# Kernel optimization log

Measured on AMD Instinct MI355X. Metric: run time of the kernel, lower is better.

The kernel has to match this reference:

```python
import jax, jax.numpy as jnp
import numpy as np

NUM_NEURON = 500_000
NUM_CONN = 8
SIM_TIME = 200
I_MAX = 20.0
FIRE_THRESHOLD = 0.5
# Izhikevich neuron parameters
THRESHOLD = 30.0
A, B, C_RESET, D = 0.02, 0.2, -65.0, 8.0
MEM0, U0 = -70.0, -14.0
DT = 0.5


def setup_inputs() -> dict:
    key = jax.random.key(0)
    k0, k1, k2, k3, k4 = jax.random.split(key, 5)
    inp = jax.random.uniform(k0, (NUM_NEURON,), jnp.float32)
    FR = jax.random.uniform(k1, (NUM_CONN, NUM_NEURON), jnp.float32)
    C = jax.random.uniform(k2, (NUM_NEURON,), jnp.float32)
    W = jax.random.normal(k3, (NUM_CONN, NUM_NEURON), jnp.float32) * 0.5
    Fired = jnp.ones((1,), jnp.float32)
    W_LatInh = jax.random.normal(k4, (NUM_NEURON,), jnp.float32)
    return {"input": inp, "FR": FR, "C": C, "Fired": Fired,
            "W_LatInh": W_LatInh, "W": W}


def _izh_spike_count(I):
    """Run SIM_TIME Izhikevich steps with constant input current I; return spike counts."""
    def step(carry, _):
        mem, u, acc = carry
        mem = mem + DT * (0.04 * mem * mem + 5.0 * mem + 140.0 - u + I)
        u = u + DT * A * (B * mem - u)
        spike = (mem >= THRESHOLD).astype(I.dtype)
        mem = spike * C_RESET + (1.0 - spike) * mem
        u = u + spike * D
        return (mem, u, acc + spike), None
    mem0 = jnp.full_like(I, MEM0)
    u0 = jnp.full_like(I, U0)
    acc0 = jnp.zeros_like(I)
    (_, _, acc), _ = jax.lax.scan(step, (mem0, u0, acc0), None, length=SIM_TIME)
    return acc


def reference(input, FR, C, Fired, W_LatInh, W):
    # weighted firing-rate sum over all input connections: [K,N] -> [N]
    FR_W = jnp.einsum('kn,kn->n', FR, W)
    sf = jnp.maximum(jnp.tanh(FR_W), 0.0)
    input_n = jnp.maximum(-C * (input - sf) + input, 0.0)
    input_r = jnp.round(input_n * I_MAX)
    spike_count = _izh_spike_count(input_r)
    FR_n = spike_count / SIM_TIME
    # binarize to detect fired neurons
    S = jnp.where(input_n >= FIRE_THRESHOLD, 1.0, 0.0)
    fired_any = (jnp.sum(S) > 0.0).astype(input.dtype)
    Fired_new = Fired + fired_any
    W_cand = jnp.tanh(W_LatInh - 2.0 * jnp.arccos(S) * jnp.exp(Fired_new) - 1.0) + 1.0
    W_LatInh_new = jnp.where(fired_any > 0.0, W_cand, W_LatInh)
    return FR_n, input_n, Fired_new, W_LatInh_new
```

## Files before the change

kernel.cpp:

```cpp
#include <hip/hip_runtime.h>


namespace {

constexpr int N    = 500000;
constexpr int NT4  = N / 4;
constexpr int BLK  = 256;
constexpr int NBLK = (NT4 + BLK - 1) / BLK;

__device__ __forceinline__ float xla_tanh(float x) {
  float xc = fminf(fmaxf(x, -9.0f), 9.0f);
  float x2 = __fmul_rn(xc, xc);
  float p = -2.76076847742355e-16f;
  p = __fadd_rn(__fmul_rn(p, x2), 2.00018790482477e-13f);
  p = __fadd_rn(__fmul_rn(p, x2), -8.60467152213735e-11f);
  p = __fadd_rn(__fmul_rn(p, x2), 5.12229709037114e-08f);
  p = __fadd_rn(__fmul_rn(p, x2), 1.48572235717979e-05f);
  p = __fadd_rn(__fmul_rn(p, x2), 6.37261928875436e-04f);
  p = __fadd_rn(__fmul_rn(p, x2), 4.89352455891786e-03f);
  p = __fmul_rn(xc, p);
  float q = 1.19825839466702e-06f;
  q = __fadd_rn(__fmul_rn(q, x2), 1.18534705686654e-04f);
  q = __fadd_rn(__fmul_rn(q, x2), 2.26843463243900e-03f);
  q = __fadd_rn(__fmul_rn(q, x2), 4.89352518554385e-03f);
  float r = p / q;
  return (fabsf(x) < 0.0004f) ? x : r;
}

__global__ void __launch_bounds__(BLK) kA(const float* __restrict__ inp,
                                          const float* __restrict__ FR,
                                          const float* __restrict__ C,
                                          const float* __restrict__ W,
                                          float* __restrict__ out,
                                          unsigned int* __restrict__ flag) {
  __shared__ float lut[24];
  const int tid = threadIdx.x;
  const int gid = blockIdx.x * BLK + tid;
  const bool active = gid < NT4;
  const int src = active ? gid : 0;

  float4 in4 = reinterpret_cast<const float4*>(inp)[src];
  float4 c4  = reinterpret_cast<const float4*>(C)[src];
  float fa[8][4], wa[8][4];
#pragma unroll
  for (int k = 0; k < 8; ++k) {
    float4 fv = reinterpret_cast<const float4*>(FR + (size_t)k * N)[src];
    float4 wv = reinterpret_cast<const float4*>(W + (size_t)k * N)[src];
    fa[k][0] = fv.x; fa[k][1] = fv.y; fa[k][2] = fv.z; fa[k][3] = fv.w;
    wa[k][0] = wv.x; wa[k][1] = wv.y; wa[k][2] = wv.z; wa[k][3] = wv.w;
  }

  if (tid < 21) {
    const float I = (float)tid;
    float mem = -70.0f, u = -14.0f, acc = 0.0f;
#pragma unroll 10
    for (int t = 0; t < 200; ++t) {
      float dm = (0.04f * mem) * mem + 5.0f * mem;
      dm = dm + 140.0f;
      dm = dm - u;
      dm = dm + I;
      mem = mem + 0.5f * dm;
      u = u + 0.01f * (0.2f * mem - u);
      const bool sp = mem >= 30.0f;
      acc += sp ? 1.0f : 0.0f;
      mem = sp ? -65.0f : mem;
      u = sp ? u + 8.0f : u;
    }
    lut[tid] = acc / 200.0f;
  }
  __syncthreads();

  if (!active) return;

  float frw[4];
#pragma unroll
  for (int j = 0; j < 4; ++j) {
    float s = __fmul_rn(fa[0][j], wa[0][j]);
#pragma unroll
    for (int k = 1; k < 8; ++k)
      s = __fadd_rn(s, __fmul_rn(fa[k][j], wa[k][j]));
    frw[j] = s;
  }

  const float iv[4] = {in4.x, in4.y, in4.z, in4.w};
  const float cv[4] = {c4.x, c4.y, c4.z, c4.w};
  float fr_n[4], in_n[4];
  bool s_any = false;
#pragma unroll
  for (int j = 0; j < 4; ++j) {
    float sf = fmaxf(xla_tanh(frw[j]), 0.0f);
    float d  = __fsub_rn(iv[j], sf);
    float v  = __fadd_rn(__fmul_rn(-cv[j], d), iv[j]);
    float n  = fmaxf(v, 0.0f);
    in_n[j] = n;
    int ir = (int)rintf(__fmul_rn(n, 20.0f));
    ir = ir < 0 ? 0 : (ir > 20 ? 20 : ir);
    fr_n[j] = lut[ir];
    s_any |= (n >= 0.5f);
  }

  float4 o0 = {fr_n[0], fr_n[1], fr_n[2], fr_n[3]};
  float4 o1 = {in_n[0], in_n[1], in_n[2], in_n[3]};
  reinterpret_cast<float4*>(out)[gid] = o0;
  reinterpret_cast<float4*>(out + N)[gid] = o1;

  unsigned long long b = __ballot(s_any);
  if (b != 0ULL && (int)(tid & 63) == (__ffsll((unsigned long long)b) - 1))
    *flag = 1u;
}

__global__ void __launch_bounds__(BLK) kB(const float* __restrict__ WLi,
                                          const float* __restrict__ Fired,
                                          const unsigned int* __restrict__ flag,
                                          float* __restrict__ out) {
  const int gid = blockIdx.x * BLK + threadIdx.x;
  const float fired_any = (*flag != 0u) ? 1.0f : 0.0f;
  const float fired_new = __fadd_rn(Fired[0], fired_any);
  if (gid == 0) out[2 * N] = fired_new;
  if (gid >= NT4) return;

  float4 wl4 = reinterpret_cast<const float4*>(WLi)[gid];
  float4 in4 = reinterpret_cast<const float4*>(out + N)[gid];
  const float wv[4] = {wl4.x, wl4.y, wl4.z, wl4.w};
  const float nv[4] = {in4.x, in4.y, in4.z, in4.w};
  float res[4];

  if (fired_any > 0.0f) {
    const float e = expf(fired_new);
#pragma unroll
    for (int j = 0; j < 4; ++j) {
      float two_acos = (nv[j] >= 0.5f) ? 0.0f : 3.14159274101257324f;
      float t = __fmul_rn(two_acos, e);
      float x = __fsub_rn(wv[j], t);
      x = __fsub_rn(x, 1.0f);
      res[j] = __fadd_rn(xla_tanh(x), 1.0f);
    }
  } else {
#pragma unroll
    for (int j = 0; j < 4; ++j) res[j] = wv[j];
  }

  float* dst = out + 2 * N + 1 + (size_t)gid * 4;
  dst[0] = res[0]; dst[1] = res[1]; dst[2] = res[2]; dst[3] = res[3];
}

}

extern "C" void kernel_launch(void* const* d_in, const int* in_sizes, int n_in,
                              void* d_out, int out_size, void* d_ws, size_t ws_size,
                              hipStream_t stream) {
  const float* inp   = (const float*)d_in[0];
  const float* FR    = (const float*)d_in[1];
  const float* C     = (const float*)d_in[2];
  const float* Fired = (const float*)d_in[3];
  const float* WLi   = (const float*)d_in[4];
  const float* W     = (const float*)d_in[5];
  float* out = (float*)d_out;
  unsigned int* flag = (unsigned int*)d_ws;

  hipMemsetAsync(flag, 0, sizeof(unsigned int), stream);
  kA<<<NBLK, BLK, 0, stream>>>(inp, FR, C, W, out, flag);
  kB<<<NBLK, BLK, 0, stream>>>(WLi, Fired, flag, out);
}
```

Baseline: 99.65 us.

## Fuse both kernels into one cooperative kernel with a grid-wide sync

Merges the main compute kernel and the lateral-inhibition update kernel into a single cooperative launch. Each block writes its own fired flag, then after a grid sync every block ORs all the flags. This removes the memset, the second launch, and the reload of input_n and W_LatInh from global memory, since the values stay in registers across the sync. In exchange it depends on all 489 blocks being co-resident, adds the cost of a grid barrier, and keeps more registers live across that barrier.

```diff
diff --git a/kernel.cpp b/kernel.cpp
--- a/kernel.cpp
+++ b/kernel.cpp
@@ -1,5 +1,8 @@
 #include <hip/hip_runtime.h>
+#include <hip/hip_cooperative_groups.h>
 
+
+namespace cg = cooperative_groups;
 
 namespace {
 
@@ -27,20 +30,27 @@
   return (fabsf(x) < 0.0004f) ? x : r;
 }
 
-__global__ void __launch_bounds__(BLK) kA(const float* __restrict__ inp,
-                                          const float* __restrict__ FR,
-                                          const float* __restrict__ C,
-                                          const float* __restrict__ W,
-                                          float* __restrict__ out,
-                                          unsigned int* __restrict__ flag) {
+__global__ void __launch_bounds__(BLK) kFused(const float* __restrict__ inp,
+                                              const float* __restrict__ FR,
+                                              const float* __restrict__ C,
+                                              const float* __restrict__ W,
+                                              const float* __restrict__ WLi,
+                                              const float* __restrict__ Fired,
+                                              float* __restrict__ out,
+                                              unsigned int* __restrict__ flags) {
   __shared__ float lut[24];
+  __shared__ unsigned int s_or;
   const int tid = threadIdx.x;
-  const int gid = blockIdx.x * BLK + tid;
+  const int bid = blockIdx.x;
+  const int gid = bid * BLK + tid;
   const bool active = gid < NT4;
   const int src = active ? gid : 0;
 
+  if (tid == 0) s_or = 0u;
+
   float4 in4 = reinterpret_cast<const float4*>(inp)[src];
   float4 c4  = reinterpret_cast<const float4*>(C)[src];
+  float4 wl4 = reinterpret_cast<const float4*>(WLi)[src];
   float fa[8][4], wa[8][4];
 #pragma unroll
   for (int k = 0; k < 8; ++k) {
@@ -70,78 +80,77 @@
   }
   __syncthreads();
 
-  if (!active) return;
-
-  float frw[4];
+  float in_n[4];
+  bool s_any = false;
+  if (active) {
+    float frw[4];
 #pragma unroll
-  for (int j = 0; j < 4; ++j) {
-    float s = __fmul_rn(fa[0][j], wa[0][j]);
+    for (int j = 0; j < 4; ++j) {
+      float s = __fmul_rn(fa[0][j], wa[0][j]);
 #pragma unroll
-    for (int k = 1; k < 8; ++k)
-      s = __fadd_rn(s, __fmul_rn(fa[k][j], wa[k][j]));
-    frw[j] = s;
+      for (int k = 1; k < 8; ++k)
+        s = __fadd_rn(s, __fmul_rn(fa[k][j], wa[k][j]));
+      frw[j] = s;
+    }
+    const float iv[4] = {in4.x, in4.y, in4.z, in4.w};
+    const float cv[4] = {c4.x, c4.y, c4.z, c4.w};
+    float fr_n[4];
+#pragma unroll
+    for (int j = 0; j < 4; ++j) {
+      float sf = fmaxf(xla_tanh(frw[j]), 0.0f);
+      float d  = __fsub_rn(iv[j], sf);
+      float v  = __fadd_rn(__fmul_rn(-cv[j], d), iv[j]);
+      float n  = fmaxf(v, 0.0f);
+      in_n[j] = n;
+      int ir = (int)rintf(__fmul_rn(n, 20.0f));
+      ir = ir < 0 ? 0 : (ir > 20 ? 20 : ir);
+      fr_n[j] = lut[ir];
+      s_any |= (n >= 0.5f);
+    }
+    float4 o0 = {fr_n[0], fr_n[1], fr_n[2], fr_n[3]};
+    float4 o1 = {in_n[0], in_n[1], in_n[2], in_n[3]};
+    reinterpret_cast<float4*>(out)[gid] = o0;
+    reinterpret_cast<float4*>(out + N)[gid] = o1;
   }
 
-  const float iv[4] = {in4.x, in4.y, in4.z, in4.w};
-  const float cv[4] = {c4.x, c4.y, c4.z, c4.w};
-  float fr_n[4], in_n[4];
-  bool s_any = false;
-#pragma unroll
-  for (int j = 0; j < 4; ++j) {
-    float sf = fmaxf(xla_tanh(frw[j]), 0.0f);
-    float d  = __fsub_rn(iv[j], sf);
-    float v  = __fadd_rn(__fmul_rn(-cv[j], d), iv[j]);
-    float n  = fmaxf(v, 0.0f);
-    in_n[j] = n;
-    int ir = (int)rintf(__fmul_rn(n, 20.0f));
-    ir = ir < 0 ? 0 : (ir > 20 ? 20 : ir);
-    fr_n[j] = lut[ir];
-    s_any |= (n >= 0.5f);
-  }
+  unsigned long long b = __ballot(s_any);
+  if ((tid & 63) == 0 && b != 0ULL) s_or = 1u;
+  __syncthreads();
+  if (tid == 0) flags[bid] = s_or;
 
-  float4 o0 = {fr_n[0], fr_n[1], fr_n[2], fr_n[3]};
-  float4 o1 = {in_n[0], in_n[1], in_n[2], in_n[3]};
-  reinterpret_cast<float4*>(out)[gid] = o0;
-  reinterpret_cast<float4*>(out + N)[gid] = o1;
+  cg::this_grid().sync();
 
-  unsigned long long b = __ballot(s_any);
-  if (b != 0ULL && (int)(tid & 63) == (__ffsll((unsigned long long)b) - 1))
-    *flag = 1u;
-}
+  unsigned int v = 0;
+  for (int i = tid; i < NBLK; i += BLK) v |= flags[i];
+  if (tid == 0) s_or = 0u;
+  __syncthreads();
+  if (v != 0u) s_or = 1u;
+  __syncthreads();
 
-__global__ void __launch_bounds__(BLK) kB(const float* __restrict__ WLi,
-                                          const float* __restrict__ Fired,
-                                          const unsigned int* __restrict__ flag,
-                                          float* __restrict__ out) {
-  const int gid = blockIdx.x * BLK + threadIdx.x;
-  const float fired_any = (*flag != 0u) ? 1.0f : 0.0f;
+  const float fired_any = s_or ? 1.0f : 0.0f;
   const float fired_new = __fadd_rn(Fired[0], fired_any);
   if (gid == 0) out[2 * N] = fired_new;
-  if (gid >= NT4) return;
 
-  float4 wl4 = reinterpret_cast<const float4*>(WLi)[gid];
-  float4 in4 = reinterpret_cast<const float4*>(out + N)[gid];
-  const float wv[4] = {wl4.x, wl4.y, wl4.z, wl4.w};
-  const float nv[4] = {in4.x, in4.y, in4.z, in4.w};
-  float res[4];
-
-  if (fired_any > 0.0f) {
-    const float e = expf(fired_new);
+  if (active) {
+    const float wv[4] = {wl4.x, wl4.y, wl4.z, wl4.w};
+    float res[4];
+    if (fired_any > 0.0f) {
+      const float e = expf(fired_new);
 #pragma unroll
-    for (int j = 0; j < 4; ++j) {
-      float two_acos = (nv[j] >= 0.5f) ? 0.0f : 3.14159274101257324f;
-      float t = __fmul_rn(two_acos, e);
-      float x = __fsub_rn(wv[j], t);
-      x = __fsub_rn(x, 1.0f);
-      res[j] = __fadd_rn(xla_tanh(x), 1.0f);
+      for (int j = 0; j < 4; ++j) {
+        float two_acos = (in_n[j] >= 0.5f) ? 0.0f : 3.14159274101257324f;
+        float t = __fmul_rn(two_acos, e);
+        float x = __fsub_rn(wv[j], t);
+        x = __fsub_rn(x, 1.0f);
+        res[j] = __fadd_rn(xla_tanh(x), 1.0f);
+      }
+    } else {
+#pragma unroll
+      for (int j = 0; j < 4; ++j) res[j] = wv[j];
     }
-  } else {
-#pragma unroll
-    for (int j = 0; j < 4; ++j) res[j] = wv[j];
+    float* dst = out + 2 * N + 1 + (size_t)gid * 4;
+    dst[0] = res[0]; dst[1] = res[1]; dst[2] = res[2]; dst[3] = res[3];
   }
-
-  float* dst = out + 2 * N + 1 + (size_t)gid * 4;
-  dst[0] = res[0]; dst[1] = res[1]; dst[2] = res[2]; dst[3] = res[3];
 }
 
 }
@@ -156,9 +165,10 @@
   const float* WLi   = (const float*)d_in[4];
   const float* W     = (const float*)d_in[5];
   float* out = (float*)d_out;
-  unsigned int* flag = (unsigned int*)d_ws;
+  unsigned int* flags = (unsigned int*)d_ws;
 
-  hipMemsetAsync(flag, 0, sizeof(unsigned int), stream);
-  kA<<<NBLK, BLK, 0, stream>>>(inp, FR, C, W, out, flag);
-  kB<<<NBLK, BLK, 0, stream>>>(WLi, Fired, flag, out);
+  void* args[] = {(void*)&inp, (void*)&FR, (void*)&C, (void*)&W,
+                  (void*)&WLi, (void*)&Fired, (void*)&out, (void*)&flags};
+  hipLaunchCooperativeKernel((const void*)kFused, dim3(NBLK), dim3(BLK),
+                             args, 0, stream);
 }
```

Result: slower. 159.7 us (+60.3%).
